# Kernel optimization log

Measured on AMD Instinct MI355X. Metric: run time of the kernel, lower is better.

Reference implementation:

```python
import jax, jax.numpy as jnp
import numpy as np

N = 8192        # number of nodes
IN_CH = 256     # in_channels
OUT_CH = 256    # out_channels


def setup_inputs() -> dict:
    key = jax.random.key(0)
    k1, k2, k3, k4 = jax.random.split(key, 4)
    A = jax.random.normal(k1, (N, N), dtype=jnp.float32)
    # degree-like matrix: only its diagonal matters; keep it strictly positive
    D = jax.random.uniform(k2, (N, N), dtype=jnp.float32, minval=0.5, maxval=2.0)
    H = jax.random.normal(k3, (N, IN_CH), dtype=jnp.float32)
    W = jax.random.normal(k4, (IN_CH, OUT_CH), dtype=jnp.float32)  # nn.Parameter, normal_() init
    return {"A": A, "D": D, "H": H, "W": W}


def reference(A, D, H, W):
    # Original: D_ = diag(diag(rsqrt(D))); T = D_ @ A @ D_ @ H @ W
    # diag-matrix matmuls are mathematically row/column scalings; same math, no O(n^3) diag mm.
    d = jax.lax.rsqrt(jnp.diagonal(D))          # [N], rsqrt of diagonal entries
    A_norm = A * d[:, None] * d[None, :]        # D^-1/2 A D^-1/2, fused elementwise
    return (A_norm @ H) @ W                     # [N, OUT_CH]
```

## Files before the change

### kernel.cpp

```cpp
#include <hip/hip_runtime.h>
#include <hip/hip_bf16.h>

#define NN 8192
#define CH 256

typedef float f32x4 __attribute__((ext_vector_type(4)));
typedef __bf16 bf16x8 __attribute__((ext_vector_type(8)));

union FragU { uint4 u; bf16x8 h; };

static __device__ __forceinline__ unsigned short f2bf(float f) {
  union { float f; unsigned int u; } v; v.f = f;
  unsigned int x = v.u;
  return (unsigned short)((x + 0x7fffu + ((x >> 16) & 1u)) >> 16);
}

#if defined(__has_builtin)
#if __has_builtin(__builtin_amdgcn_global_load_lds)
#define HAVE_GLL 1
#endif
#endif

#ifdef HAVE_GLL
static __device__ __forceinline__ void gload16(const void* g, void* l) {
  __builtin_amdgcn_global_load_lds(
      (const __attribute__((address_space(1))) void*)(unsigned long long)(g),
      (__attribute__((address_space(3))) void*)(unsigned int)(unsigned long long)(l),
      16, 0, 0);
}
#endif

static __device__ __forceinline__ unsigned int cvtpk(float a, float b) {
  unsigned int r;
  asm("v_cvt_pk_bf16_f32 %0, %1, %2" : "=v"(r) : "v"(a), "v"(b));
  return r;
}

#define WAITV(n) asm volatile("s_waitcnt vmcnt(" #n ")" ::: "memory")
#define BARRIER() __builtin_amdgcn_s_barrier()

__global__ __launch_bounds__(256) void k_prep(const float* __restrict__ Hm,
                                              const float* __restrict__ Dm,
                                              const float* __restrict__ Wm,
                                              unsigned short* __restrict__ HT,
                                              unsigned short* __restrict__ WT) {
  __shared__ float tile[64][65];
  int bx = blockIdx.x, t = threadIdx.x;
  bool isH = bx < 512;
  int b = isH ? bx : bx - 512;
  int r0 = (b >> 2) * 64;
  int j0 = (b & 3) * 64;
  const float* src = isH ? Hm : Wm;

  int r = t >> 2;
  int cq = (t & 3) * 16;
  float dval = isH ? rsqrtf(Dm[(size_t)(r0 + r) * (NN + 1)]) : 1.0f;
  const float* p = src + (size_t)(r0 + r) * CH + j0 + cq;
#pragma unroll
  for (int u = 0; u < 4; ++u) {
    float4 v = *(const float4*)(p + u * 4);
    tile[r][cq + u * 4 + 0] = v.x * dval;
    tile[r][cq + u * 4 + 1] = v.y * dval;
    tile[r][cq + u * 4 + 2] = v.z * dval;
    tile[r][cq + u * 4 + 3] = v.w * dval;
  }
  __syncthreads();
  int j = t >> 2;
  int kq = (t & 3) * 16;
  __align__(16) unsigned short ov[16];
#pragma unroll
  for (int i = 0; i < 16; ++i) ov[i] = f2bf(tile[kq + i][j]);
  unsigned short* dst = isH ? (HT + (size_t)(j0 + j) * NN + r0 + kq)
                            : (WT + (size_t)(j0 + j) * CH + r0 + kq);
  *(uint4*)dst = *(uint4*)ov;
  *(uint4*)(dst + 8) = *(uint4*)(ov + 8);
}

__global__ __launch_bounds__(512, 1) void k_fused(const float* __restrict__ A,
                                                  const float* __restrict__ Dm,
                                                  const unsigned short* __restrict__ HT,
                                                  const unsigned short* __restrict__ WT,
                                                  float* __restrict__ out) {
  constexpr int NIT = NN / 64;
  __shared__ float Asf[2][2048];
  __shared__ unsigned short Gs[32][264];
  __shared__ float dsh[32];
  const int bx = blockIdx.x, t = threadIdx.x, l = t & 63, w = t >> 6;
  const int lan = l & 15, quad = l >> 4;
  const int i0 = bx * 32;

  const char* Ag = (const char*)A + (size_t)(i0 + (t >> 4)) * NN * 4
                   + (size_t)(((t & 15) ^ ((t >> 4) & 7)) * 16);
  const unsigned short* Bb = HT + (size_t)(w * 32 + lan) * NN + quad * 8;

  if (t < 32) dsh[t] = rsqrtf(Dm[(size_t)(i0 + t) * (NN + 1)]);

  FragU b0[4], b1[4];
  f32x4 acc[2][2];
#pragma unroll
  for (int mt = 0; mt < 2; ++mt)
#pragma unroll
    for (int nt = 0; nt < 2; ++nt)
#pragma unroll
      for (int c = 0; c < 4; ++c) acc[mt][nt][c] = 0.0f;

  auto stage = [&](int kt, int buf) {
#ifdef HAVE_GLL
    gload16(Ag + (size_t)kt * 256, (char*)&Asf[buf][0] + t * 16);
#else
    float4 tv = *(const float4*)(Ag + (size_t)kt * 256);
    *(float4*)((char*)&Asf[buf][0] + t * 16) = tv;
    asm volatile("s_waitcnt lgkmcnt(0)" ::: "memory");
#endif
  };

  auto loadB = [&](FragU (&dst)[4], int kt) {
    const unsigned short* p = Bb + (size_t)kt * 64;
#pragma unroll
    for (int ss = 0; ss < 2; ++ss)
#pragma unroll
      for (int nt = 0; nt < 2; ++nt)
        dst[ss * 2 + nt].u = *(const uint4*)(p + (size_t)nt * 16 * NN + ss * 32);
  };

  const int sw = (lan & 7) * 16;
  auto compute = [&](FragU (&b)[4], const char* Ab) {
#pragma unroll
    for (int ss = 0; ss < 2; ++ss) {
      FragU af[2];
#pragma unroll
      for (int mt = 0; mt < 2; ++mt) {
        const char* rp = Ab + (mt * 16 + lan) * 256;
        const int x = ss * 128 + quad * 32;
        float4 va = *(const float4*)(rp + ((x) ^ sw));
        float4 vb = *(const float4*)(rp + ((x + 16) ^ sw));
        af[mt].u.x = cvtpk(va.x, va.y);
        af[mt].u.y = cvtpk(va.z, va.w);
        af[mt].u.z = cvtpk(vb.x, vb.y);
        af[mt].u.w = cvtpk(vb.z, vb.w);
      }
#pragma unroll
      for (int mt = 0; mt < 2; ++mt)
#pragma unroll
        for (int nt = 0; nt < 2; ++nt)
          acc[mt][nt] = __builtin_amdgcn_mfma_f32_16x16x32_bf16(af[mt].h, b[ss * 2 + nt].h,
                                                                acc[mt][nt], 0, 0, 0);
    }
  };

  stage(0, 0);
  loadB(b0, 0);
#pragma unroll 1
  for (int kt = 0; kt < NIT; kt += 2) {
    stage(kt + 1, 1);
    loadB(b1, kt + 1);
    WAITV(5);
    BARRIER();
    compute(b0, (const char*)&Asf[0][0]);
    BARRIER();
    if (kt + 2 < NIT) {
      stage(kt + 2, 0);
      loadB(b0, kt + 2);
      WAITV(5);
    } else {
      WAITV(0);
    }
    BARRIER();
    compute(b1, (const char*)&Asf[1][0]);
    BARRIER();
  }

#pragma unroll
  for (int mt = 0; mt < 2; ++mt)
#pragma unroll
    for (int nt = 0; nt < 2; ++nt)
#pragma unroll
      for (int r = 0; r < 4; ++r) {
        const int row = mt * 16 + quad * 4 + r;
        Gs[row][w * 32 + nt * 16 + lan] = f2bf(acc[mt][nt][r] * dsh[row]);
      }
  __syncthreads();

  const int r0w = (w & 1) * 16, j0c = (w >> 1) * 64;
  f32x4 o[4];
#pragma unroll
  for (int nt = 0; nt < 4; ++nt)
#pragma unroll
    for (int c = 0; c < 4; ++c) o[nt][c] = 0.0f;
#pragma unroll
  for (int ks = 0; ks < 8; ++ks) {
    FragU af;
    af.u = *(const uint4*)&Gs[r0w + lan][ks * 32 + quad * 8];
#pragma unroll
    for (int nt = 0; nt < 4; ++nt) {
      FragU bw;
      bw.u = *(const uint4*)&WT[(size_t)(j0c + nt * 16 + lan) * CH + ks * 32 + quad * 8];
      o[nt] = __builtin_amdgcn_mfma_f32_16x16x32_bf16(af.h, bw.h, o[nt], 0, 0, 0);
    }
  }
#pragma unroll
  for (int nt = 0; nt < 4; ++nt)
#pragma unroll
    for (int r = 0; r < 4; ++r)
      out[(size_t)(i0 + r0w + quad * 4 + r) * CH + j0c + nt * 16 + lan] = o[nt][r];
}

extern "C" void kernel_launch(void* const* d_in, const int* in_sizes, int n_in,
                              void* d_out, int out_size, void* d_ws, size_t ws_size,
                              hipStream_t stream) {
  const float* A  = (const float*)d_in[0];
  const float* Dm = (const float*)d_in[1];
  const float* Hm = (const float*)d_in[2];
  const float* Wm = (const float*)d_in[3];
  float* out = (float*)d_out;
  char* ws = (char*)d_ws;
  unsigned short* HT = (unsigned short*)ws;
  unsigned short* WT = (unsigned short*)(ws + (size_t)4194304);

  hipLaunchKernelGGL(k_prep, dim3(528), dim3(256), 0, stream, Hm, Dm, Wm, HT, WT);
  hipLaunchKernelGGL(k_fused, dim3(256), dim3(512), 0, stream, A, Dm, HT, WT, out);
}
```

Before: 580.2 us.

## Stage A through registers, convert to bf16 before LDS, 4-deep ring buffer

Replaces the direct global-to-LDS fp32 load of A with register-staged loads that are converted to bf16 once and written into a 4-slot swizzled LDS ring. This halves LDS footprint and read traffic per tile, removes per-wave redundant conversion work in the compute loop, and cuts barriers from two to one per k-step thanks to the deeper ring. It adds register pressure, manual vmcnt accounting, and a hand-written pipeline epilogue that must stay correct.

Measured after the change: 543.4 us. 6.3% less time.

```diff
diff --git a/kernel.cpp b/kernel.cpp
--- a/kernel.cpp
+++ b/kernel.cpp
@@ -15,21 +15,6 @@
   return (unsigned short)((x + 0x7fffu + ((x >> 16) & 1u)) >> 16);
 }
 
-#if defined(__has_builtin)
-#if __has_builtin(__builtin_amdgcn_global_load_lds)
-#define HAVE_GLL 1
-#endif
-#endif
-
-#ifdef HAVE_GLL
-static __device__ __forceinline__ void gload16(const void* g, void* l) {
-  __builtin_amdgcn_global_load_lds(
-      (const __attribute__((address_space(1))) void*)(unsigned long long)(g),
-      (__attribute__((address_space(3))) void*)(unsigned int)(unsigned long long)(l),
-      16, 0, 0);
-}
-#endif
-
 static __device__ __forceinline__ unsigned int cvtpk(float a, float b) {
   unsigned int r;
   asm("v_cvt_pk_bf16_f32 %0, %1, %2" : "=v"(r) : "v"(a), "v"(b));
@@ -37,7 +22,9 @@
 }
 
 #define WAITV(n) asm volatile("s_waitcnt vmcnt(" #n ")" ::: "memory")
+#define LGKM0()  asm volatile("s_waitcnt lgkmcnt(0)" ::: "memory")
 #define BARRIER() __builtin_amdgcn_s_barrier()
+#define FENCE()  asm volatile("" ::: "memory")
 
 __global__ __launch_bounds__(256) void k_prep(const float* __restrict__ Hm,
                                               const float* __restrict__ Dm,
@@ -82,20 +69,22 @@
                                                   const unsigned short* __restrict__ WT,
                                                   float* __restrict__ out) {
   constexpr int NIT = NN / 64;
-  __shared__ float Asf[2][2048];
+  __shared__ unsigned short Asb[4][2048];
   __shared__ unsigned short Gs[32][264];
   __shared__ float dsh[32];
-  const int bx = blockIdx.x, t = threadIdx.x, l = t & 63, w = t >> 6;
+  const int t = threadIdx.x, l = t & 63, w = t >> 6;
   const int lan = l & 15, quad = l >> 4;
-  const int i0 = bx * 32;
-
-  const char* Ag = (const char*)A + (size_t)(i0 + (t >> 4)) * NN * 4
-                   + (size_t)(((t & 15) ^ ((t >> 4) & 7)) * 16);
+  const int i0 = blockIdx.x * 32;
+
+  const int arow = t >> 4;
+  const int aswr = arow * 64 + (((t & 15) * 4) ^ ((arow & 7) * 8));
+  const char* Ag = (const char*)A + (size_t)(i0 + arow) * NN * 4 + (t & 15) * 16;
   const unsigned short* Bb = HT + (size_t)(w * 32 + lan) * NN + quad * 8;
 
   if (t < 32) dsh[t] = rsqrtf(Dm[(size_t)(i0 + t) * (NN + 1)]);
 
-  FragU b0[4], b1[4];
+  FragU bb0[4], bb1[4];
+  float4 aS0, aS1;
   f32x4 acc[2][2];
 #pragma unroll
   for (int mt = 0; mt < 2; ++mt)
@@ -104,16 +93,15 @@
 #pragma unroll
       for (int c = 0; c < 4; ++c) acc[mt][nt][c] = 0.0f;
 
-  auto stage = [&](int kt, int buf) {
-#ifdef HAVE_GLL
-    gload16(Ag + (size_t)kt * 256, (char*)&Asf[buf][0] + t * 16);
-#else
-    float4 tv = *(const float4*)(Ag + (size_t)kt * 256);
-    *(float4*)((char*)&Asf[buf][0] + t * 16) = tv;
-    asm volatile("s_waitcnt lgkmcnt(0)" ::: "memory");
-#endif
-  };
-
+  auto aload = [&](float4& dst, int kt) {
+    dst = *(const float4*)(Ag + (size_t)kt * 256);
+  };
+  auto cvtwrite = [&](const float4& v, int bi) {
+    uint2 pk;
+    pk.x = cvtpk(v.x, v.y);
+    pk.y = cvtpk(v.z, v.w);
+    *(uint2*)&Asb[bi][aswr] = pk;
+  };
   auto loadB = [&](FragU (&dst)[4], int kt) {
     const unsigned short* p = Bb + (size_t)kt * 64;
 #pragma unroll
@@ -122,22 +110,14 @@
       for (int nt = 0; nt < 2; ++nt)
         dst[ss * 2 + nt].u = *(const uint4*)(p + (size_t)nt * 16 * NN + ss * 32);
   };
-
-  const int sw = (lan & 7) * 16;
-  auto compute = [&](FragU (&b)[4], const char* Ab) {
+  auto compute = [&](FragU (&b)[4], const unsigned short* Ab) {
 #pragma unroll
     for (int ss = 0; ss < 2; ++ss) {
       FragU af[2];
 #pragma unroll
       for (int mt = 0; mt < 2; ++mt) {
-        const char* rp = Ab + (mt * 16 + lan) * 256;
-        const int x = ss * 128 + quad * 32;
-        float4 va = *(const float4*)(rp + ((x) ^ sw));
-        float4 vb = *(const float4*)(rp + ((x + 16) ^ sw));
-        af[mt].u.x = cvtpk(va.x, va.y);
-        af[mt].u.y = cvtpk(va.z, va.w);
-        af[mt].u.z = cvtpk(vb.x, vb.y);
-        af[mt].u.w = cvtpk(vb.z, vb.w);
+        const int row = mt * 16 + lan;
+        af[mt].u = *(const uint4*)&Ab[row * 64 + ((ss * 32 + quad * 8) ^ ((lan & 7) * 8))];
       }
 #pragma unroll
       for (int mt = 0; mt < 2; ++mt)
@@ -148,28 +128,57 @@
     }
   };
 
-  stage(0, 0);
-  loadB(b0, 0);
+  aload(aS0, 0);
+  aload(aS1, 1);
+  loadB(bb0, 0);
+  WAITV(5);
+  cvtwrite(aS0, 0);
+  aload(aS0, 2);
+
 #pragma unroll 1
-  for (int kt = 0; kt < NIT; kt += 2) {
-    stage(kt + 1, 1);
-    loadB(b1, kt + 1);
-    WAITV(5);
-    BARRIER();
-    compute(b0, (const char*)&Asf[0][0]);
-    BARRIER();
-    if (kt + 2 < NIT) {
-      stage(kt + 2, 0);
-      loadB(b0, kt + 2);
-      WAITV(5);
-    } else {
-      WAITV(0);
-    }
-    BARRIER();
-    compute(b1, (const char*)&Asf[1][0]);
-    BARRIER();
-  }
-
+  for (int kt = 0; kt + 5 < NIT; kt += 2) {
+    WAITV(5);
+    cvtwrite(aS1, (kt + 1) & 3);
+    loadB(bb1, kt + 1);
+    aload(aS1, kt + 3);
+    WAITV(6);
+    LGKM0(); BARRIER(); FENCE();
+    compute(bb0, &Asb[kt & 3][0]);
+    WAITV(5);
+    cvtwrite(aS0, (kt + 2) & 3);
+    loadB(bb0, kt + 2);
+    aload(aS0, kt + 4);
+    WAITV(6);
+    LGKM0(); BARRIER(); FENCE();
+    compute(bb1, &Asb[(kt + 1) & 3][0]);
+  }
+
+  {
+    WAITV(5);
+    cvtwrite(aS1, (NIT - 3) & 3);
+    loadB(bb1, NIT - 3);
+    aload(aS1, NIT - 1);
+    WAITV(6);
+    LGKM0(); BARRIER(); FENCE();
+    compute(bb0, &Asb[(NIT - 4) & 3][0]);
+    WAITV(5);
+    cvtwrite(aS0, (NIT - 2) & 3);
+    loadB(bb0, NIT - 2);
+    WAITV(5);
+    LGKM0(); BARRIER(); FENCE();
+    compute(bb1, &Asb[(NIT - 3) & 3][0]);
+    WAITV(4);
+    cvtwrite(aS1, (NIT - 1) & 3);
+    loadB(bb1, NIT - 1);
+    WAITV(4);
+    LGKM0(); BARRIER(); FENCE();
+    compute(bb0, &Asb[(NIT - 2) & 3][0]);
+    WAITV(0);
+    LGKM0(); BARRIER(); FENCE();
+    compute(bb1, &Asb[(NIT - 1) & 3][0]);
+  }
+
+  LGKM0(); BARRIER(); FENCE();
 #pragma unroll
   for (int mt = 0; mt < 2; ++mt)
 #pragma unroll
```
